# Optimization experiments

Hardware: AMD Instinct MI355X
Metric: run time of the kernel (lower is better)

Reference implementation:

```python
import jax, jax.numpy as jnp
import numpy as np

B, N, D, H = 256, 256, 136, 128  # queries, docs/query, feature dim, hidden dim


def setup_inputs() -> dict:
    key = jax.random.key(0)
    ks = jax.random.split(key, 7)
    features = jax.random.uniform(ks[0], (B, N, D), dtype=jnp.float32)
    labels = jax.random.randint(ks[1], (B, N), 0, 5, dtype=jnp.int32)  # relevance grades 0..4
    # Small init scales keep MLP scores in (-1, 1) so log2(1 + max(s_i, s_j)) is well-defined
    W1 = jax.random.normal(ks[2], (D, H), dtype=jnp.float32) * 0.05
    b1 = jnp.zeros((H,), dtype=jnp.float32)
    W2 = jax.random.normal(ks[3], (H, H), dtype=jnp.float32) * 0.05
    b2 = jnp.zeros((H,), dtype=jnp.float32)
    W3 = jax.random.normal(ks[4], (H, 1), dtype=jnp.float32) * 0.02
    b3 = jnp.zeros((1,), dtype=jnp.float32)
    return {"features": features, "labels": labels,
            "W1": W1, "b1": b1, "W2": W2, "b2": b2, "W3": W3, "b3": b3}


def _scores(features, W1, b1, W2, b2, W3, b3):
    # Linear-ReLU-(Dropout: identity in eval)-Linear-ReLU-Linear, then squeeze(-1)
    h = jax.nn.relu(jnp.einsum('bnd,dh->bnh', features, W1) + b1)
    h = jax.nn.relu(jnp.einsum('bnh,hk->bnk', h, W2) + b2)
    return (jnp.einsum('bnh,ho->bno', h, W3) + b3).squeeze(-1)  # [B, N]


def _compute_lambdas(scores, labels):
    si = scores[:, :, None]        # s_i  [B, N, 1]
    sj = scores[:, None, :]        # s_j  [B, 1, N]
    li = labels[:, :, None]
    lj = labels[:, None, :]
    # lambda_ij = 0.5 * (1 - sigmoid(s_j - s_i)) = 0.5 * sigmoid(s_i - s_j)
    lam = 0.5 * jax.nn.sigmoid(si - sj)
    gain = jnp.exp2(labels.astype(scores.dtype))  # 2 ** l
    dndcg = jnp.abs((gain[:, :, None] - gain[:, None, :])
                    / (1.0 + jnp.log2(1.0 + jnp.maximum(si, sj))))
    A = jnp.where(li > lj, lam * dndcg, jnp.zeros((), scores.dtype))  # [B, N, N]
    # lambdas[i] += A[i, j] over j (pairs where l_i > l_j); lambdas[j] -= A[i, j]
    return A.sum(-1) - A.sum(-2)  # [B, N]


def reference(features, labels, W1, b1, W2, b2, W3, b3):
    scores = _scores(features, W1, b1, W2, b2, W3, b3)
    return _compute_lambdas(scores, labels)
```

## Files before the change

kernel.cpp:

```cpp
#include <hip/hip_runtime.h>
#include <hip/hip_bf16.h>

#define DIN  136
#define HH   128
#define NSEQ 256
#define NB   256
#define ST   136

typedef __attribute__((ext_vector_type(4))) float f32x4;
typedef __attribute__((ext_vector_type(8))) short bf16x8;

static __device__ __forceinline__ unsigned cvt2(float lo, float hi) {
    __hip_bfloat162 h = __float22bfloat162_rn(make_float2(lo, hi));
    return *(unsigned*)&h;
}
static __device__ __forceinline__ short f2bf1(float f) {
    __hip_bfloat16 h = __float2bfloat16(f);
    return *(short*)&h;
}

__global__ __launch_bounds__(256)
void prep_kernel(const float* __restrict__ W1, const float* __restrict__ W2,
                 short* __restrict__ w1s, short* __restrict__ w2s)
{
    const int nt = gridDim.x * 256;
    const int idx = blockIdx.x * 256 + threadIdx.x;
    for (int e = idx; e < HH * ST; e += nt) {
        const int n = e / ST, k = e - n * ST;
        w1s[e] = f2bf1(W1[k * HH + n]);
    }
    for (int e = idx; e < HH * ST; e += nt) {
        const int n = e / ST, k = e - n * ST;
        w2s[e] = (k < HH) ? f2bf1(W2[k * HH + n]) : (short)0;
    }
}

__global__ __launch_bounds__(1024, 4)
void fused_kernel(const float* __restrict__ features,
                  const int*   __restrict__ labels,
                  const short* __restrict__ w1s,
                  const short* __restrict__ w2s,
                  const float* __restrict__ b1, const float* __restrict__ b2,
                  const float* __restrict__ W3, const float* __restrict__ b3,
                  float* __restrict__ out)
{
    __shared__ __align__(16) char smem[139264];
    short* a_lds  = (short*)smem;
    short* w1_lds = (short*)(smem + 69632);
    short* w2_lds = (short*)(smem + 104448);
    float4* sp    = (float4*)smem;
    float (*s_part)[NSEQ] = (float (*)[NSEQ])(smem + 4096);

    const int t    = threadIdx.x;
    const int lane = t & 63;
    const int wv   = t >> 6;
    const int l15  = lane & 15;
    const int l4   = lane >> 4;
    const long row0 = (long)blockIdx.x * NSEQ;

    {
        const uint4* src = (const uint4*)w1s;
        uint4* dst = (uint4*)w1_lds;
        for (int i = t; i < 2 * HH * ST / 8; i += 1024)
            dst[i] = src[i];
    }
    {
        const f32x4* src = (const f32x4*)(features + row0 * DIN);
        for (int i = t; i < NSEQ * DIN / 4; i += 1024) {
            const f32x4 v = src[i];
            const int r = i / 34, c = i - r * 34;
            uint2 p;
            p.x = cvt2(v.x, v.y);
            p.y = cvt2(v.z, v.w);
            *(uint2*)&a_lds[r * ST + c * 4] = p;
        }
    }
    __syncthreads();

    const int arow = (wv * 16 + l15) * ST;

    f32x4 acc[8];
#pragma unroll
    for (int tn = 0; tn < 8; ++tn) {
        const float bv = b1[tn * 16 + l15];
        acc[tn] = (f32x4){bv, bv, bv, bv};
    }
    for (int kc = 0; kc < 4; ++kc) {
        const int kb = kc * 32 + l4 * 8;
        const bf16x8 afr = *(const bf16x8*)&a_lds[arow + kb];
        bf16x8 bfr[8];
#pragma unroll
        for (int tn = 0; tn < 8; ++tn)
            bfr[tn] = *(const bf16x8*)&w1_lds[(tn * 16 + l15) * ST + kb];
#pragma unroll
        for (int tn = 0; tn < 8; ++tn)
            acc[tn] = __builtin_amdgcn_mfma_f32_16x16x32_bf16(afr, bfr[tn], acc[tn], 0, 0, 0);
    }
    {
        bf16x8 afr = (bf16x8){0,0,0,0,0,0,0,0};
        bf16x8 bfr[8];
#pragma unroll
        for (int tn = 0; tn < 8; ++tn) bfr[tn] = (bf16x8){0,0,0,0,0,0,0,0};
        if (l4 == 0) {
            afr = *(const bf16x8*)&a_lds[arow + 128];
#pragma unroll
            for (int tn = 0; tn < 8; ++tn)
                bfr[tn] = *(const bf16x8*)&w1_lds[(tn * 16 + l15) * ST + 128];
        }
#pragma unroll
        for (int tn = 0; tn < 8; ++tn)
            acc[tn] = __builtin_amdgcn_mfma_f32_16x16x32_bf16(afr, bfr[tn], acc[tn], 0, 0, 0);
    }

#pragma unroll
    for (int tn = 0; tn < 8; ++tn) {
        const int col = tn * 16 + l15;
#pragma unroll
        for (int j = 0; j < 4; ++j)
            a_lds[(wv * 16 + l4 * 4 + j) * ST + col] = f2bf1(fmaxf(acc[tn][j], 0.f));
    }

    f32x4 acc2[8];
#pragma unroll
    for (int tn = 0; tn < 8; ++tn) {
        const float bv = b2[tn * 16 + l15];
        acc2[tn] = (f32x4){bv, bv, bv, bv};
    }
    for (int kc = 0; kc < 4; ++kc) {
        const int kb = kc * 32 + l4 * 8;
        const bf16x8 afr = *(const bf16x8*)&a_lds[arow + kb];
        bf16x8 bfr[8];
#pragma unroll
        for (int tn = 0; tn < 8; ++tn)
            bfr[tn] = *(const bf16x8*)&w2_lds[(tn * 16 + l15) * ST + kb];
#pragma unroll
        for (int tn = 0; tn < 8; ++tn)
            acc2[tn] = __builtin_amdgcn_mfma_f32_16x16x32_bf16(afr, bfr[tn], acc2[tn], 0, 0, 0);
    }
    __syncthreads();

    {
        float w3v[8];
#pragma unroll
        for (int tn = 0; tn < 8; ++tn) w3v[tn] = W3[tn * 16 + l15];
        const float b3v = b3[0];
#pragma unroll
        for (int j = 0; j < 4; ++j) {
            float p = 0.f;
#pragma unroll
            for (int tn = 0; tn < 8; ++tn)
                p += fmaxf(acc2[tn][j], 0.f) * w3v[tn];
            p += __shfl_xor(p, 1, 64);
            p += __shfl_xor(p, 2, 64);
            p += __shfl_xor(p, 4, 64);
            p += __shfl_xor(p, 8, 64);
            if (l15 == 0) {
                const int row = wv * 16 + l4 * 4 + j;
                const float s = p + b3v;
                const int lab = labels[row0 + row];
                const float g = 0.5f * exp2f((float)lab);
                const float disc = 1.f / (1.f + log2f(1.f + s));
                sp[row] = make_float4(s * 1.44269504088896f,
                                      g, disc, 0.f);
            }
        }
    }
    __syncthreads();

    {
        const int i  = t & (NSEQ - 1);
        const int jg = t >> 8;
        const float4 me = sp[i];
        const float sci = me.x, gi = me.y, di = me.z;
        float accum = 0.f;
        const int j0 = jg * 64;
#pragma unroll 8
        for (int jj = 0; jj < 64; ++jj) {
            const float4 o = sp[j0 + jj];
            const float dg = o.y - gi;
            const float e  = exp2f(o.x - sci);
            const float r  = __builtin_amdgcn_rcpf(1.f + e);
            const float dmax = (sci > o.x) ? di : o.z;
            const float dn = fabsf(dg) * dmax;
            const float w  = (dg < 0.f) ? r : (r - 1.f);
            accum += dn * w;
        }
        s_part[jg][i] = accum;
    }
    __syncthreads();
    {
        const int i = t & (NSEQ - 1);
        if ((t >> 8) == 0)
            out[row0 + i] = s_part[0][i] + s_part[1][i] +
                            s_part[2][i] + s_part[3][i];
    }
}

extern "C" void kernel_launch(void* const* d_in, const int* in_sizes, int n_in,
                              void* d_out, int out_size, void* d_ws, size_t ws_size,
                              hipStream_t stream)
{
    const float* features = (const float*)d_in[0];
    const int*   labels   = (const int*)d_in[1];
    const float* W1 = (const float*)d_in[2];
    const float* b1 = (const float*)d_in[3];
    const float* W2 = (const float*)d_in[4];
    const float* b2 = (const float*)d_in[5];
    const float* W3 = (const float*)d_in[6];
    const float* b3 = (const float*)d_in[7];

    short* w1s = (short*)d_ws;
    short* w2s = w1s + HH * ST;
    float* out = (float*)d_out;

    prep_kernel<<<64, 256, 0, stream>>>(W1, W2, w1s, w2s);
    fused_kernel<<<NB, 1024, 0, stream>>>(
        features, labels, w1s, w2s, b1, b2, W3, b3, out);
}
```

Measured before the change: 106.0 us.

## Use 32x32x16 MFMA on half the waves and batch global loads into registers

The MLP matmuls switch from 16x16x32 to 32x32x16 bf16 MFMA, so only 8 of 16 waves each compute a 32-row tile, which cuts LDS fragment reloads of the weights. Feature and W1 loads are first issued into registers all at once and then converted and written to LDS, exposing more memory-level parallelism than the strided loop. The cost is that half the waves sit idle during the GEMMs, and each MFMA wave carries more accumulator registers.

```diff
diff --git a/kernel.cpp b/kernel.cpp
--- a/kernel.cpp
+++ b/kernel.cpp
@@ -7,8 +7,9 @@
 #define NB   256
 #define ST   136
 
-typedef __attribute__((ext_vector_type(4))) float f32x4;
-typedef __attribute__((ext_vector_type(8))) short bf16x8;
+typedef __attribute__((ext_vector_type(4)))  float f32x4;
+typedef __attribute__((ext_vector_type(16))) float f32x16;
+typedef __attribute__((ext_vector_type(8)))  short bf16x8;
 
 static __device__ __forceinline__ unsigned cvt2(float lo, float hi) {
     __hip_bfloat162 h = __float22bfloat162_rn(make_float2(lo, hi));
@@ -54,108 +55,133 @@
     const int t    = threadIdx.x;
     const int lane = t & 63;
     const int wv   = t >> 6;
-    const int l15  = lane & 15;
-    const int l4   = lane >> 4;
     const long row0 = (long)blockIdx.x * NSEQ;
 
+    const f32x4* fsrc = (const f32x4*)(features + row0 * DIN);
+    f32x4 fg[8];
+#pragma unroll
+    for (int m = 0; m < 8; ++m) fg[m] = fsrc[t + m * 1024];
+    f32x4 fg8 = {};
+    if (t < 512) fg8 = fsrc[8192 + t];
+
+    const uint4* wsrc = (const uint4*)w1s;
+    uint4 wg[4];
+#pragma unroll
+    for (int m = 0; m < 4; ++m) wg[m] = wsrc[t + m * 1024];
+    uint4 wg4 = {};
+    if (t < 256) wg4 = wsrc[4096 + t];
+
+#pragma unroll
+    for (int m = 0; m < 8; ++m) {
+        const int i = t + m * 1024;
+        const int r = i / 34, c = i - r * 34;
+        uint2 p; p.x = cvt2(fg[m].x, fg[m].y); p.y = cvt2(fg[m].z, fg[m].w);
+        *(uint2*)&a_lds[r * ST + c * 4] = p;
+    }
+    if (t < 512) {
+        const int i = 8192 + t;
+        const int r = i / 34, c = i - r * 34;
+        uint2 p; p.x = cvt2(fg8.x, fg8.y); p.y = cvt2(fg8.z, fg8.w);
+        *(uint2*)&a_lds[r * ST + c * 4] = p;
+    }
     {
-        const uint4* src = (const uint4*)w1s;
-        uint4* dst = (uint4*)w1_lds;
-        for (int i = t; i < 2 * HH * ST / 8; i += 1024)
-            dst[i] = src[i];
-    }
-    {
-        const f32x4* src = (const f32x4*)(features + row0 * DIN);
-        for (int i = t; i < NSEQ * DIN / 4; i += 1024) {
-            const f32x4 v = src[i];
-            const int r = i / 34, c = i - r * 34;
-            uint2 p;
-            p.x = cvt2(v.x, v.y);
-            p.y = cvt2(v.z, v.w);
-            *(uint2*)&a_lds[r * ST + c * 4] = p;
-        }
-    }
-    __syncthreads();
-
-    const int arow = (wv * 16 + l15) * ST;
-
-    f32x4 acc[8];
-#pragma unroll
-    for (int tn = 0; tn < 8; ++tn) {
-        const float bv = b1[tn * 16 + l15];
-        acc[tn] = (f32x4){bv, bv, bv, bv};
-    }
-    for (int kc = 0; kc < 4; ++kc) {
-        const int kb = kc * 32 + l4 * 8;
-        const bf16x8 afr = *(const bf16x8*)&a_lds[arow + kb];
-        bf16x8 bfr[8];
-#pragma unroll
-        for (int tn = 0; tn < 8; ++tn)
-            bfr[tn] = *(const bf16x8*)&w1_lds[(tn * 16 + l15) * ST + kb];
-#pragma unroll
-        for (int tn = 0; tn < 8; ++tn)
-            acc[tn] = __builtin_amdgcn_mfma_f32_16x16x32_bf16(afr, bfr[tn], acc[tn], 0, 0, 0);
-    }
-    {
-        bf16x8 afr = (bf16x8){0,0,0,0,0,0,0,0};
-        bf16x8 bfr[8];
-#pragma unroll
-        for (int tn = 0; tn < 8; ++tn) bfr[tn] = (bf16x8){0,0,0,0,0,0,0,0};
-        if (l4 == 0) {
-            afr = *(const bf16x8*)&a_lds[arow + 128];
-#pragma unroll
-            for (int tn = 0; tn < 8; ++tn)
-                bfr[tn] = *(const bf16x8*)&w1_lds[(tn * 16 + l15) * ST + 128];
-        }
-#pragma unroll
-        for (int tn = 0; tn < 8; ++tn)
-            acc[tn] = __builtin_amdgcn_mfma_f32_16x16x32_bf16(afr, bfr[tn], acc[tn], 0, 0, 0);
-    }
-
-#pragma unroll
-    for (int tn = 0; tn < 8; ++tn) {
-        const int col = tn * 16 + l15;
-#pragma unroll
-        for (int j = 0; j < 4; ++j)
-            a_lds[(wv * 16 + l4 * 4 + j) * ST + col] = f2bf1(fmaxf(acc[tn][j], 0.f));
-    }
-
-    f32x4 acc2[8];
-#pragma unroll
-    for (int tn = 0; tn < 8; ++tn) {
-        const float bv = b2[tn * 16 + l15];
-        acc2[tn] = (f32x4){bv, bv, bv, bv};
-    }
-    for (int kc = 0; kc < 4; ++kc) {
-        const int kb = kc * 32 + l4 * 8;
-        const bf16x8 afr = *(const bf16x8*)&a_lds[arow + kb];
-        bf16x8 bfr[8];
-#pragma unroll
-        for (int tn = 0; tn < 8; ++tn)
-            bfr[tn] = *(const bf16x8*)&w2_lds[(tn * 16 + l15) * ST + kb];
-#pragma unroll
-        for (int tn = 0; tn < 8; ++tn)
-            acc2[tn] = __builtin_amdgcn_mfma_f32_16x16x32_bf16(afr, bfr[tn], acc2[tn], 0, 0, 0);
-    }
-    __syncthreads();
-
-    {
-        float w3v[8];
-#pragma unroll
-        for (int tn = 0; tn < 8; ++tn) w3v[tn] = W3[tn * 16 + l15];
+        uint4* wdst = (uint4*)w1_lds;
+#pragma unroll
+        for (int m = 0; m < 4; ++m) wdst[t + m * 1024] = wg[m];
+        if (t < 256) wdst[4096 + t] = wg4;
+    }
+    __syncthreads();
+
+    f32x16 acc2[4];
+    const int l31 = lane & 31;
+    const int kg  = lane >> 5;
+    if (t < 512) {
+        const int mw   = wv;
+        const int arow = (mw * 32 + l31) * ST;
+
+        f32x16 acc[4];
+#pragma unroll
+        for (int tn = 0; tn < 4; ++tn) {
+            const float bv = b1[tn * 32 + l31];
+#pragma unroll
+            for (int q = 0; q < 16; ++q) acc[tn][q] = bv;
+        }
+        for (int kc = 0; kc < 8; ++kc) {
+            const int kb = kc * 16 + kg * 8;
+            const bf16x8 afr = *(const bf16x8*)&a_lds[arow + kb];
+            bf16x8 bfr[4];
+#pragma unroll
+            for (int tn = 0; tn < 4; ++tn)
+                bfr[tn] = *(const bf16x8*)&w1_lds[(tn * 32 + l31) * ST + kb];
+#pragma unroll
+            for (int tn = 0; tn < 4; ++tn)
+                acc[tn] = __builtin_amdgcn_mfma_f32_32x32x16_bf16(afr, bfr[tn], acc[tn], 0, 0, 0);
+        }
+        {
+            bf16x8 afr = (bf16x8){0,0,0,0,0,0,0,0};
+            bf16x8 bfr[4];
+#pragma unroll
+            for (int tn = 0; tn < 4; ++tn) bfr[tn] = (bf16x8){0,0,0,0,0,0,0,0};
+            if (kg == 0) {
+                afr = *(const bf16x8*)&a_lds[arow + 128];
+#pragma unroll
+                for (int tn = 0; tn < 4; ++tn)
+                    bfr[tn] = *(const bf16x8*)&w1_lds[(tn * 32 + l31) * ST + 128];
+            }
+#pragma unroll
+            for (int tn = 0; tn < 4; ++tn)
+                acc[tn] = __builtin_amdgcn_mfma_f32_32x32x16_bf16(afr, bfr[tn], acc[tn], 0, 0, 0);
+        }
+
+#pragma unroll
+        for (int tn = 0; tn < 4; ++tn) {
+            const int n = tn * 32 + l31;
+#pragma unroll
+            for (int q = 0; q < 16; ++q) {
+                const int R = mw * 32 + (q & 3) + 8 * (q >> 2) + 4 * kg;
+                a_lds[R * ST + n] = f2bf1(fmaxf(acc[tn][q], 0.f));
+            }
+        }
+
+#pragma unroll
+        for (int tn = 0; tn < 4; ++tn) {
+            const float bv = b2[tn * 32 + l31];
+#pragma unroll
+            for (int q = 0; q < 16; ++q) acc2[tn][q] = bv;
+        }
+        for (int kc = 0; kc < 8; ++kc) {
+            const int kb = kc * 16 + kg * 8;
+            const bf16x8 afr = *(const bf16x8*)&a_lds[arow + kb];
+            bf16x8 bfr[4];
+#pragma unroll
+            for (int tn = 0; tn < 4; ++tn)
+                bfr[tn] = *(const bf16x8*)&w2_lds[(tn * 32 + l31) * ST + kb];
+#pragma unroll
+            for (int tn = 0; tn < 4; ++tn)
+                acc2[tn] = __builtin_amdgcn_mfma_f32_32x32x16_bf16(afr, bfr[tn], acc2[tn], 0, 0, 0);
+        }
+    }
+    __syncthreads();
+
+    if (t < 512) {
+        const int mw = wv;
+        float w3v[4];
+#pragma unroll
+        for (int tn = 0; tn < 4; ++tn) w3v[tn] = W3[tn * 32 + l31];
         const float b3v = b3[0];
 #pragma unroll
-        for (int j = 0; j < 4; ++j) {
+        for (int q = 0; q < 16; ++q) {
             float p = 0.f;
 #pragma unroll
-            for (int tn = 0; tn < 8; ++tn)
-                p += fmaxf(acc2[tn][j], 0.f) * w3v[tn];
+            for (int tn = 0; tn < 4; ++tn)
+                p += fmaxf(acc2[tn][q], 0.f) * w3v[tn];
             p += __shfl_xor(p, 1, 64);
             p += __shfl_xor(p, 2, 64);
             p += __shfl_xor(p, 4, 64);
             p += __shfl_xor(p, 8, 64);
-            if (l15 == 0) {
-                const int row = wv * 16 + l4 * 4 + j;
+            p += __shfl_xor(p, 16, 64);
+            if (l31 == 0) {
+                const int row = mw * 32 + (q & 3) + 8 * (q >> 2) + 4 * kg;
                 const float s = p + b3v;
                 const int lab = labels[row0 + row];
                 const float g = 0.5f * exp2f((float)lab);
```

Result: no change. 107.0 us (+0.9%).

## Pre-convert features to bf16 and stage into LDS via global_load_lds

Applied to the files above, without the earlier changes.

The prep kernel now converts the whole feature tensor to bf16 in workspace, and the fused kernel copies features and weights straight into LDS with direct global-to-LDS loads, skipping register staging and in-kernel conversion. Score staging buffers move to a separate LDS region, allowing one barrier to be removed. The trade-off is an extra write and re-read of the features through global memory, which increases total memory traffic.

```diff
diff --git a/kernel.cpp b/kernel.cpp
--- a/kernel.cpp
+++ b/kernel.cpp
@@ -10,6 +10,9 @@
 typedef __attribute__((ext_vector_type(4))) float f32x4;
 typedef __attribute__((ext_vector_type(8))) short bf16x8;
 
+typedef const __attribute__((address_space(1))) unsigned int gas_u32;
+typedef __attribute__((address_space(3))) unsigned int las_u32;
+
 static __device__ __forceinline__ unsigned cvt2(float lo, float hi) {
     __hip_bfloat162 h = __float22bfloat162_rn(make_float2(lo, hi));
     return *(unsigned*)&h;
@@ -18,38 +21,52 @@
     __hip_bfloat16 h = __float2bfloat16(f);
     return *(short*)&h;
 }
+static __device__ __forceinline__ void gld_lds16(const void* g, void* l) {
+    __builtin_amdgcn_global_load_lds((gas_u32*)g, (las_u32*)l, 16, 0, 0);
+}
 
 __global__ __launch_bounds__(256)
-void prep_kernel(const float* __restrict__ W1, const float* __restrict__ W2,
-                 short* __restrict__ w1s, short* __restrict__ w2s)
+void prep_kernel(const float* __restrict__ features,
+                 const float* __restrict__ W1, const float* __restrict__ W2,
+                 short* __restrict__ wbuf,
+                 unsigned* __restrict__ fbf)
 {
     const int nt = gridDim.x * 256;
     const int idx = blockIdx.x * 256 + threadIdx.x;
     for (int e = idx; e < HH * ST; e += nt) {
         const int n = e / ST, k = e - n * ST;
-        w1s[e] = f2bf1(W1[k * HH + n]);
+        wbuf[e] = f2bf1(W1[k * HH + n]);
     }
     for (int e = idx; e < HH * ST; e += nt) {
         const int n = e / ST, k = e - n * ST;
-        w2s[e] = (k < HH) ? f2bf1(W2[k * HH + n]) : (short)0;
+        wbuf[HH * ST + e] = (k < HH) ? f2bf1(W2[k * HH + n]) : (short)0;
+    }
+    const f32x4* src = (const f32x4*)features;
+    uint2* dst = (uint2*)fbf;
+    const int total = NB * NSEQ * DIN / 4;
+    for (int i = idx; i < total; i += nt) {
+        const f32x4 v = src[i];
+        uint2 p;
+        p.x = cvt2(v.x, v.y);
+        p.y = cvt2(v.z, v.w);
+        dst[i] = p;
     }
 }
 
 __global__ __launch_bounds__(1024, 4)
-void fused_kernel(const float* __restrict__ features,
+void fused_kernel(const short* __restrict__ wbuf,
+                  const short* __restrict__ fbf,
                   const int*   __restrict__ labels,
-                  const short* __restrict__ w1s,
-                  const short* __restrict__ w2s,
                   const float* __restrict__ b1, const float* __restrict__ b2,
                   const float* __restrict__ W3, const float* __restrict__ b3,
                   float* __restrict__ out)
 {
-    __shared__ __align__(16) char smem[139264];
+    __shared__ __align__(16) char smem[147456];
     short* a_lds  = (short*)smem;
     short* w1_lds = (short*)(smem + 69632);
     short* w2_lds = (short*)(smem + 104448);
-    float4* sp    = (float4*)smem;
-    float (*s_part)[NSEQ] = (float (*)[NSEQ])(smem + 4096);
+    float4* sp    = (float4*)(smem + 139264);
+    float (*s_part)[NSEQ] = (float (*)[NSEQ])(smem + 143360);
 
     const int t    = threadIdx.x;
     const int lane = t & 63;
@@ -59,21 +76,13 @@
     const long row0 = (long)blockIdx.x * NSEQ;
 
     {
-        const uint4* src = (const uint4*)w1s;
-        uint4* dst = (uint4*)w1_lds;
-        for (int i = t; i < 2 * HH * ST / 8; i += 1024)
-            dst[i] = src[i];
-    }
-    {
-        const f32x4* src = (const f32x4*)(features + row0 * DIN);
-        for (int i = t; i < NSEQ * DIN / 4; i += 1024) {
-            const f32x4 v = src[i];
-            const int r = i / 34, c = i - r * 34;
-            uint2 p;
-            p.x = cvt2(v.x, v.y);
-            p.y = cvt2(v.z, v.w);
-            *(uint2*)&a_lds[r * ST + c * 4] = p;
-        }
+        const char* fsrc = (const char*)fbf + (size_t)blockIdx.x * 69632;
+        const char* wsrc = (const char*)wbuf;
+        const int lo = lane * 16;
+        for (int c = wv; c < 68; c += 16)
+            gld_lds16(fsrc + c * 1024 + lo, smem + c * 1024 + lo);
+        for (int c = wv; c < 68; c += 16)
+            gld_lds16(wsrc + c * 1024 + lo, smem + 69632 + c * 1024 + lo);
     }
     __syncthreads();
 
@@ -137,7 +146,6 @@
         for (int tn = 0; tn < 8; ++tn)
             acc2[tn] = __builtin_amdgcn_mfma_f32_16x16x32_bf16(afr, bfr[tn], acc2[tn], 0, 0, 0);
     }
-    __syncthreads();
 
     {
         float w3v[8];
@@ -185,7 +193,7 @@
             const float w  = (dg < 0.f) ? r : (r - 1.f);
             accum += dn * w;
         }
-        s_part[jg][i] = accum;
+        s_part[jg][t & 255] = accum;
     }
     __syncthreads();
     {
@@ -209,11 +217,11 @@
     const float* W3 = (const float*)d_in[6];
     const float* b3 = (const float*)d_in[7];
 
-    short* w1s = (short*)d_ws;
-    short* w2s = w1s + HH * ST;
-    float* out = (float*)d_out;
-
-    prep_kernel<<<64, 256, 0, stream>>>(W1, W2, w1s, w2s);
+    short*    wbuf = (short*)d_ws;
+    unsigned* fbf  = (unsigned*)(wbuf + 2 * HH * ST);
+    float*    out  = (float*)d_out;
+
+    prep_kernel<<<2048, 256, 0, stream>>>(features, W1, W2, wbuf, fbf);
     fused_kernel<<<NB, 1024, 0, stream>>>(
-        features, labels, w1s, w2s, b1, b2, W3, b3, out);
-}
+        wbuf, (const short*)fbf, labels, b1, b2, W3, b3, out);
+}
```

New measurement: 112.1 us. 5.8% more time.
